# Performance work log

Hardware: AMD Instinct MI355X
Metric: run time of the kernel (lower is better)

The kernel has to match this reference:

```python
import jax, jax.numpy as jnp
import numpy as np

SINKHORN_ITERS = 100
SINKHORN_EPS = 0.1
M, N, D = 2048, 2048, 512


def setup_inputs() -> dict:
    key = jax.random.key(0)
    k1, k2 = jax.random.split(key)
    d_M_q = jax.random.normal(k1, (M, D), dtype=jnp.float32)
    d_N_r = jax.random.normal(k2, (N, D), dtype=jnp.float32)
    # upstream pipeline applies F.normalize(p=2, dim=1) before matching;
    # unit-norm rows keep scores in [-1, 1] so exp(score/0.1) is finite
    d_M_q = d_M_q / jnp.linalg.norm(d_M_q, axis=1, keepdims=True)
    d_N_r = d_N_r / jnp.linalg.norm(d_N_r, axis=1, keepdims=True)
    z = jnp.float32(0.5)  # learned SuperGlue bin_score (default init)
    return {"d_M_q": d_M_q, "d_N_r": d_N_r, "z": z}


def reference(d_M_q, d_N_r, z):
    m, n = d_M_q.shape[0], d_N_r.shape[0]
    score = d_M_q @ d_N_r.T                        # [M, N]
    # augmented matrix: scores in top-left block, dustbin row/col/corner = z
    S_aug = jnp.full((m + 1, n + 1), z, dtype=d_M_q.dtype)
    S_aug = S_aug.at[:m, :n].set(score)            # [M+1, N+1]
    K = jnp.exp(S_aug / SINKHORN_EPS)

    def body(K, _):
        K = K / jnp.sum(K, axis=1, keepdims=True)  # row normalize
        K = K / jnp.sum(K, axis=0, keepdims=True)  # col normalize
        return K, None

    K, _ = jax.lax.scan(body, K, None, length=SINKHORN_ITERS)
    P = K[:m, :n]
    return P, K
```

## Files before the change

kernel.cpp:

```cpp
#include <hip/hip_runtime.h>
#include <hip/hip_fp16.h>

#define MM 2048
#define NN 2048
#define DD 512
#define NA 2049
#define LDH 2056
#define LDE 1024
#define ITERS 100
#define NWG 257
#define TPB 512

typedef __attribute__((ext_vector_type(8))) short short8;
typedef __attribute__((ext_vector_type(4))) float f32x4;

__device__ __forceinline__ unsigned short f2bf(float x) {
    unsigned u = __builtin_bit_cast(unsigned, x);
    u += 0x7FFFu + ((u >> 16) & 1u);
    return (unsigned short)(u >> 16);
}
__device__ __forceinline__ float bf2f(unsigned short h) {
    unsigned u = ((unsigned)h) << 16;
    return __builtin_bit_cast(float, u);
}
__device__ __forceinline__ void gload_lds16(const void* g, void* l) {
    __builtin_amdgcn_global_load_lds(
        (const __attribute__((address_space(1))) void*)g,
        (__attribute__((address_space(3))) void*)l, 16, 0, 0);
}

__global__ __launch_bounds__(256) void init_fill(float* __restrict__ Kreg,
                                                 _Float16* __restrict__ K0h,
                                                 float* __restrict__ c,
                                                 unsigned* __restrict__ ctrl,
                                                 const float* __restrict__ zp) {
    int t = blockIdx.x * 256 + threadIdx.x;
    float e5 = expf(zp[0] * 10.0f);
    if (t < 512) ctrl[t] = 0u;
    if (t < NA) {
        c[t] = 1.0f;
        Kreg[(size_t)2048 * NA + t] = e5;
        K0h[(size_t)2048 * LDH + t] = (_Float16)e5;
    }
    if (t < MM) {
        Kreg[(size_t)t * NA + 2048] = e5;
        K0h[(size_t)t * LDH + 2048] = (_Float16)e5;
    }
}

__global__ __launch_bounds__(256) void split_bf16(const float* __restrict__ Q,
                                                  const float* __restrict__ Rm,
                                                  ushort* __restrict__ Qe,
                                                  ushort* __restrict__ Re) {
    const float* src = blockIdx.y ? Rm : Q;
    ushort* dst = blockIdx.y ? Re : Qe;
    int e4 = blockIdx.x * 256 + threadIdx.x;
    int row = e4 >> 7;
    int c4 = (e4 & 127) * 4;
    float4 v = *(const float4*)(src + (size_t)row * DD + c4);
    ushort4 hi, lo;
    hi.x = f2bf(v.x); lo.x = f2bf(v.x - bf2f(hi.x));
    hi.y = f2bf(v.y); lo.y = f2bf(v.y - bf2f(hi.y));
    hi.z = f2bf(v.z); lo.z = f2bf(v.z - bf2f(hi.z));
    hi.w = f2bf(v.w); lo.w = f2bf(v.w - bf2f(hi.w));
    *(ushort4*)(dst + (size_t)row * LDE + c4) = hi;
    *(ushort4*)(dst + (size_t)row * LDE + 512 + c4) = lo;
}

__global__ __launch_bounds__(256, 2) void gemm_mfma(const ushort* __restrict__ Ae,
                                                    const ushort* __restrict__ Be,
                                                    float* __restrict__ Kreg,
                                                    _Float16* __restrict__ K0h) {
    __shared__ ushort Als[64 * 32];
    __shared__ ushort Bls[128 * 32];
    const int tid = threadIdx.x;
    const int wid = tid >> 6, lane = tid & 63;
    const int row0 = blockIdx.y * 64, col0 = blockIdx.x * 128;
    const int wr = wid >> 1, wc = wid & 1;

    const int sr = lane >> 2, sc = (lane & 3) * 8;
    const ushort* gA  = Ae + (size_t)(row0 + wid * 16 + sr) * LDE + sc;
    const ushort* gB0 = Be + (size_t)(col0 + wid * 16 + sr) * LDE + sc;
    const ushort* gB1 = Be + (size_t)(col0 + 64 + wid * 16 + sr) * LDE + sc;
    ushort* lA  = &Als[wid * 16 * 32];
    ushort* lB0 = &Bls[wid * 16 * 32];
    ushort* lB1 = &Bls[(64 + wid * 16) * 32];

    f32x4 acc[2][4] = {};
    const int fr = lane & 15, fk = (lane >> 4) * 8;

    for (int k0 = 0; k0 < 1024; k0 += 32) {
        __syncthreads();
        gload_lds16(gA + k0, lA);
        gload_lds16(gB0 + k0, lB0);
        gload_lds16(gB1 + k0, lB1);
        __syncthreads();
        short8 a[2], b[4];
#pragma unroll
        for (int mi = 0; mi < 2; ++mi)
            a[mi] = *(const short8*)&Als[(wr * 32 + mi * 16 + fr) * 32 + fk];
#pragma unroll
        for (int ni = 0; ni < 4; ++ni)
            b[ni] = *(const short8*)&Bls[(wc * 64 + ni * 16 + fr) * 32 + fk];
#pragma unroll
        for (int mi = 0; mi < 2; ++mi)
#pragma unroll
            for (int ni = 0; ni < 4; ++ni)
                acc[mi][ni] = __builtin_amdgcn_mfma_f32_16x16x32_bf16(
                    a[mi], b[ni], acc[mi][ni], 0, 0, 0);
    }

#pragma unroll
    for (int mi = 0; mi < 2; ++mi)
#pragma unroll
        for (int ni = 0; ni < 4; ++ni)
#pragma unroll
            for (int q = 0; q < 4; ++q) {
                int row = row0 + wr * 32 + mi * 16 + (lane >> 4) * 4 + q;
                int col = col0 + wc * 64 + ni * 16 + fr;
                float v = expf(acc[mi][ni][q] * 10.0f);
                Kreg[(size_t)row * NA + col] = v;
                K0h[(size_t)row * LDH + col] = (_Float16)v;
            }
}

__global__ __launch_bounds__(256) void transpose_h(const _Float16* __restrict__ src,
                                                   _Float16* __restrict__ dst) {
    __shared__ _Float16 t[64][65];
    const int x0 = blockIdx.x * 64, y0 = blockIdx.y * 64;
    const int lx = threadIdx.x & 63, lyb = threadIdx.x >> 6;
    for (int ly = lyb; ly < 64; ly += 4) {
        int y = y0 + ly, x = x0 + lx;
        if (y < NA && x < NA) t[ly][lx] = src[(size_t)y * LDH + x];
    }
    __syncthreads();
    for (int ly = lyb; ly < 64; ly += 4) {
        int y = x0 + ly, x = y0 + lx;
        if (y < NA && x < NA) dst[(size_t)y * LDH + x] = t[lx][ly];
    }
}

__device__ __forceinline__ void grid_barrier(unsigned* slot) {
    __syncthreads();
    if (threadIdx.x == 0) {
        __hip_atomic_fetch_add(slot, 1u, __ATOMIC_ACQ_REL, __HIP_MEMORY_SCOPE_AGENT);
        while (__hip_atomic_load(slot, __ATOMIC_ACQUIRE, __HIP_MEMORY_SCOPE_AGENT)
               != (unsigned)NWG)
            __builtin_amdgcn_s_sleep(1);
    }
    __syncthreads();
}

__device__ __forceinline__ float rowdot(const _Float16* __restrict__ Krow,
                                        const float* v, int lane) {
    float sum = 0.0f;
#pragma unroll
    for (int s = 0; s < 4; ++s) {
        const int j = (s * 64 + lane) * 8;
        union { uint4 u; _Float16 h[8]; } kv;
        kv.u = *(const uint4*)(Krow + j);
        float4 c0 = *(const float4*)(v + j);
        float4 c1 = *(const float4*)(v + j + 4);
        sum += (float)kv.h[0] * c0.x + (float)kv.h[1] * c0.y +
               (float)kv.h[2] * c0.z + (float)kv.h[3] * c0.w +
               (float)kv.h[4] * c1.x + (float)kv.h[5] * c1.y +
               (float)kv.h[6] * c1.z + (float)kv.h[7] * c1.w;
    }
    if (lane == 0) sum += (float)Krow[2048] * v[2048];
#pragma unroll
    for (int off = 32; off; off >>= 1) sum += __shfl_xor(sum, off, 64);
    return sum;
}

__global__ __launch_bounds__(TPB) void sinkhorn_persist(
    const _Float16* __restrict__ K0h, const _Float16* __restrict__ K0hT,
    float* r, float* c, unsigned* slots, unsigned* chg)
{
    const int wave = threadIdx.x >> 6, lane = threadIdx.x & 63;
    const int row = blockIdx.x * 8 + wave;
    const bool active = row < NA;
    const _Float16* KrowA = K0h  + (size_t)row * LDH;
    const _Float16* KrowB = K0hT + (size_t)row * LDH;
    __shared__ int ls_chg, ls_exit;
    float c_prev = 1.0f;

    for (int it = 0; it < ITERS; ++it) {
        if (threadIdx.x == 0) ls_chg = 0;
        if (active) {
            float s = rowdot(KrowA, c, lane);
            if (lane == 0) r[row] = 1.0f / s;
        }
        grid_barrier(&slots[2 * it]);
        float cv = 0.0f;
        if (active) {
            float s = rowdot(KrowB, r, lane);
            cv = 1.0f / s;
            if (lane == 0) c[row] = cv;
        }
        if (active && lane == 0) {
            if (fabsf(cv - c_prev) > 1e-6f * fabsf(c_prev)) ls_chg = 1;
            c_prev = cv;
        }
        __syncthreads();
        if (threadIdx.x == 0 && ls_chg)
            __hip_atomic_fetch_or(&chg[it], 1u, __ATOMIC_RELAXED,
                                  __HIP_MEMORY_SCOPE_AGENT);
        grid_barrier(&slots[2 * it + 1]);
        if (threadIdx.x == 0)
            ls_exit = (__hip_atomic_load(&chg[it], __ATOMIC_RELAXED,
                                         __HIP_MEMORY_SCOPE_AGENT) == 0u);
        __syncthreads();
        if (ls_exit) break;
    }
}

__global__ __launch_bounds__(256) void finalize(const float* __restrict__ r,
                                                const float* __restrict__ c,
                                                float* __restrict__ Kreg,
                                                float* __restrict__ P) {
    const int row = blockIdx.x;
    const float rs = r[row];
    for (int col = threadIdx.x; col < NA; col += 256) {
        float v = Kreg[(size_t)row * NA + col] * rs * c[col];
        Kreg[(size_t)row * NA + col] = v;
        if (row < MM && col < NN) P[(size_t)row * NN + col] = v;
    }
}

extern "C" void kernel_launch(void* const* d_in, const int* in_sizes, int n_in,
                              void* d_out, int out_size, void* d_ws, size_t ws_size,
                              hipStream_t stream) {
    const float* Q  = (const float*)d_in[0];
    const float* Rm = (const float*)d_in[1];
    const float* zp = (const float*)d_in[2];

    float* P    = (float*)d_out;
    float* Kreg = P + (size_t)MM * NN;

    ushort* Qe = (ushort*)d_out;
    ushort* Re = Qe + (size_t)2048 * LDE;

    char* ws = (char*)d_ws;
    const size_t HBYTES = 8425728;
    _Float16* K0h  = (_Float16*)ws;
    _Float16* K0hT = (_Float16*)(ws + HBYTES);
    float* c = (float*)(ws + 2 * HBYTES);
    float* r = c + 2560;
    unsigned* ctrl = (unsigned*)(r + 2560);
    unsigned* slots = ctrl;
    unsigned* chg   = ctrl + 256;

    init_fill<<<dim3(9), dim3(256), 0, stream>>>(Kreg, K0h, c, ctrl, zp);
    split_bf16<<<dim3(1024, 2), dim3(256), 0, stream>>>(Q, Rm, Qe, Re);
    gemm_mfma<<<dim3(16, 32), dim3(256), 0, stream>>>(Qe, Re, Kreg, K0h);
    transpose_h<<<dim3(33, 33), dim3(256), 0, stream>>>(K0h, K0hT);
    sinkhorn_persist<<<dim3(NWG), dim3(TPB), 0, stream>>>(K0h, K0hT, r, c, slots, chg);
    finalize<<<dim3(2049), dim3(256), 0, stream>>>(r, c, Kreg, P);
}
```

Before: 120.0 us.

## Fuse init into split kernel and write transposed K directly from GEMM epilogue

```diff
diff --git a/kernel.cpp b/kernel.cpp
--- a/kernel.cpp
+++ b/kernel.cpp
@@ -29,48 +29,53 @@
         (__attribute__((address_space(3))) void*)l, 16, 0, 0);
 }
 
-__global__ __launch_bounds__(256) void init_fill(float* __restrict__ Kreg,
-                                                 _Float16* __restrict__ K0h,
-                                                 float* __restrict__ c,
-                                                 unsigned* __restrict__ ctrl,
-                                                 const float* __restrict__ zp) {
-    int t = blockIdx.x * 256 + threadIdx.x;
-    float e5 = expf(zp[0] * 10.0f);
-    if (t < 512) ctrl[t] = 0u;
-    if (t < NA) {
-        c[t] = 1.0f;
-        Kreg[(size_t)2048 * NA + t] = e5;
-        K0h[(size_t)2048 * LDH + t] = (_Float16)e5;
-    }
-    if (t < MM) {
-        Kreg[(size_t)t * NA + 2048] = e5;
-        K0h[(size_t)t * LDH + 2048] = (_Float16)e5;
-    }
-}
-
-__global__ __launch_bounds__(256) void split_bf16(const float* __restrict__ Q,
+__global__ __launch_bounds__(256) void init_split(const float* __restrict__ Q,
                                                   const float* __restrict__ Rm,
                                                   ushort* __restrict__ Qe,
-                                                  ushort* __restrict__ Re) {
-    const float* src = blockIdx.y ? Rm : Q;
-    ushort* dst = blockIdx.y ? Re : Qe;
-    int e4 = blockIdx.x * 256 + threadIdx.x;
-    int row = e4 >> 7;
-    int c4 = (e4 & 127) * 4;
-    float4 v = *(const float4*)(src + (size_t)row * DD + c4);
-    ushort4 hi, lo;
-    hi.x = f2bf(v.x); lo.x = f2bf(v.x - bf2f(hi.x));
-    hi.y = f2bf(v.y); lo.y = f2bf(v.y - bf2f(hi.y));
-    hi.z = f2bf(v.z); lo.z = f2bf(v.z - bf2f(hi.z));
-    hi.w = f2bf(v.w); lo.w = f2bf(v.w - bf2f(hi.w));
-    *(ushort4*)(dst + (size_t)row * LDE + c4) = hi;
-    *(ushort4*)(dst + (size_t)row * LDE + 512 + c4) = lo;
+                                                  ushort* __restrict__ Re,
+                                                  float* __restrict__ Kreg,
+                                                  _Float16* __restrict__ K0h,
+                                                  _Float16* __restrict__ K0hT,
+                                                  float* __restrict__ c,
+                                                  unsigned* __restrict__ ctrl,
+                                                  const float* __restrict__ zp) {
+    if (blockIdx.x < 1024) {
+        const float* src = blockIdx.y ? Rm : Q;
+        ushort* dst = blockIdx.y ? Re : Qe;
+        int e4 = blockIdx.x * 256 + threadIdx.x;
+        int row = e4 >> 7;
+        int c4 = (e4 & 127) * 4;
+        float4 v = *(const float4*)(src + (size_t)row * DD + c4);
+        ushort4 hi, lo;
+        hi.x = f2bf(v.x); lo.x = f2bf(v.x - bf2f(hi.x));
+        hi.y = f2bf(v.y); lo.y = f2bf(v.y - bf2f(hi.y));
+        hi.z = f2bf(v.z); lo.z = f2bf(v.z - bf2f(hi.z));
+        hi.w = f2bf(v.w); lo.w = f2bf(v.w - bf2f(hi.w));
+        *(ushort4*)(dst + (size_t)row * LDE + c4) = hi;
+        *(ushort4*)(dst + (size_t)row * LDE + 512 + c4) = lo;
+    } else {
+        float e5 = expf(zp[0] * 10.0f);
+        int idx = (blockIdx.x - 1024) * 512 + blockIdx.y * 256 + threadIdx.x;
+        for (int t = idx; t < NA; t += 1024) {
+            if (t < 512) ctrl[t] = 0u;
+            c[t] = 1.0f;
+            Kreg[(size_t)2048 * NA + t] = e5;
+            K0h [(size_t)2048 * LDH + t] = (_Float16)e5;
+            K0hT[(size_t)2048 * LDH + t] = (_Float16)e5;
+            if (t < MM) {
+                Kreg[(size_t)t * NA + 2048] = e5;
+                K0h [(size_t)t * LDH + 2048] = (_Float16)e5;
+                K0hT[(size_t)t * LDH + 2048] = (_Float16)e5;
+            }
+        }
+    }
 }
 
 __global__ __launch_bounds__(256, 2) void gemm_mfma(const ushort* __restrict__ Ae,
                                                     const ushort* __restrict__ Be,
                                                     float* __restrict__ Kreg,
-                                                    _Float16* __restrict__ K0h) {
+                                                    _Float16* __restrict__ K0h,
+                                                    _Float16* __restrict__ K0hT) {
     __shared__ ushort Als[64 * 32];
     __shared__ ushort Bls[128 * 32];
     const int tid = threadIdx.x;
@@ -113,31 +118,20 @@
 #pragma unroll
     for (int mi = 0; mi < 2; ++mi)
 #pragma unroll
-        for (int ni = 0; ni < 4; ++ni)
+        for (int ni = 0; ni < 4; ++ni) {
+            const int rowb = row0 + wr * 32 + mi * 16 + (lane >> 4) * 4;
+            const int col  = col0 + wc * 64 + ni * 16 + fr;
+            union { ushort4 u; _Float16 h[4]; } tp;
 #pragma unroll
             for (int q = 0; q < 4; ++q) {
-                int row = row0 + wr * 32 + mi * 16 + (lane >> 4) * 4 + q;
-                int col = col0 + wc * 64 + ni * 16 + fr;
                 float v = expf(acc[mi][ni][q] * 10.0f);
-                Kreg[(size_t)row * NA + col] = v;
-                K0h[(size_t)row * LDH + col] = (_Float16)v;
+                Kreg[(size_t)(rowb + q) * NA + col] = v;
+                _Float16 hv = (_Float16)v;
+                K0h[(size_t)(rowb + q) * LDH + col] = hv;
+                tp.h[q] = hv;
             }
-}
-
-__global__ __launch_bounds__(256) void transpose_h(const _Float16* __restrict__ src,
-                                                   _Float16* __restrict__ dst) {
-    __shared__ _Float16 t[64][65];
-    const int x0 = blockIdx.x * 64, y0 = blockIdx.y * 64;
-    const int lx = threadIdx.x & 63, lyb = threadIdx.x >> 6;
-    for (int ly = lyb; ly < 64; ly += 4) {
-        int y = y0 + ly, x = x0 + lx;
-        if (y < NA && x < NA) t[ly][lx] = src[(size_t)y * LDH + x];
-    }
-    __syncthreads();
-    for (int ly = lyb; ly < 64; ly += 4) {
-        int y = x0 + ly, x = y0 + lx;
-        if (y < NA && x < NA) dst[(size_t)y * LDH + x] = t[lx][ly];
-    }
+            *(ushort4*)(K0hT + (size_t)col * LDH + rowb) = tp.u;
+        }
 }
 
 __device__ __forceinline__ void grid_barrier(unsigned* slot) {
@@ -250,10 +244,10 @@
     unsigned* slots = ctrl;
     unsigned* chg   = ctrl + 256;
 
-    init_fill<<<dim3(9), dim3(256), 0, stream>>>(Kreg, K0h, c, ctrl, zp);
-    split_bf16<<<dim3(1024, 2), dim3(256), 0, stream>>>(Q, Rm, Qe, Re);
-    gemm_mfma<<<dim3(16, 32), dim3(256), 0, stream>>>(Qe, Re, Kreg, K0h);
-    transpose_h<<<dim3(33, 33), dim3(256), 0, stream>>>(K0h, K0hT);
-    sinkhorn_persist<<<dim3(NWG), dim3(TPB), 0, stream>>>(K0h, K0hT, r, c, slots, chg);
+    init_split<<<dim3(1026, 2), dim3(256), 0, stream>>>(Q, Rm, Qe, Re, Kreg,
+                                                        K0h, K0hT, c, ctrl, zp);
+    gemm_mfma<<<dim3(16, 32), dim3(256), 0, stream>>>(Qe, Re, Kreg, K0h, K0hT);
+    sinkhorn_persist<<<dim3(NWG), dim3(TPB), 0, stream>>>(K0h, K0hT, r, c,
+                                                          slots, chg);
     finalize<<<dim3(2049), dim3(256), 0, stream>>>(r, c, Kreg, P);
 }
```

New measurement: 109.9 us. 8.4% less time.
